# Kernel tuning notes

Hardware: AMD Instinct MI355X
Metric: run time of the kernel (lower is better)

Reference implementation:

```python
import jax, jax.numpy as jnp
import numpy as np

N_NODES = 50000
NEG_SLOPE = 0.2  # PyG GATConv default leaky-relu slope


def _gat_conv(x, edge_index, W, a_src, a_dst, bias, heads, out_ch, concat, num_nodes):
    # x: [N, F_in]; W: [F_in, heads*out_ch]; a_src/a_dst: [heads, out_ch]; bias: [heads*out_ch] or [out_ch]
    h = (x @ W).reshape(num_nodes, heads, out_ch)            # [N,H,C]
    alpha_src = jnp.einsum('nhc,hc->nh', h, a_src)           # [N,H]
    alpha_dst = jnp.einsum('nhc,hc->nh', h, a_dst)           # [N,H]
    src, dst = edge_index[0], edge_index[1]
    e = jax.nn.leaky_relu(alpha_src[src] + alpha_dst[dst], NEG_SLOPE)  # [E,H]
    # segment softmax over incoming edges per destination (self-loops guarantee non-empty segments)
    m = jax.ops.segment_max(e, dst, num_segments=num_nodes)
    e = jnp.exp(e - m[dst])
    denom = jax.ops.segment_sum(e, dst, num_segments=num_nodes)
    alpha = e / denom[dst]                                    # [E,H]
    msg = h[src] * alpha[:, :, None]                          # [E,H,C]
    out = jax.ops.segment_sum(msg, dst, num_segments=num_nodes)  # [N,H,C]
    if concat:
        out = out.reshape(num_nodes, heads * out_ch)
    else:
        out = out.mean(axis=1)
    return out + bias


def _add_self_loops(edge_index, num_nodes):
    loops = jnp.arange(num_nodes, dtype=edge_index.dtype)
    return jnp.concatenate([edge_index, jnp.stack([loops, loops])], axis=1)


def setup_inputs() -> dict:
    key = jax.random.key(0)
    ks = jax.random.split(key, 16)
    N, F_in, H, C_hid, C_out = N_NODES, 128, 4, 64, 64
    E = 800000
    x = jax.random.normal(ks[0], (N, F_in), dtype=jnp.float32)
    edge_index = jax.random.randint(ks[1], (2, E), 0, N, dtype=jnp.int32)
    s = lambda fan: 1.0 / np.sqrt(fan)
    inp = {
        'x': x, 'edge_index': edge_index,
        'W1': jax.random.normal(ks[2], (F_in, H * C_hid), jnp.float32) * s(F_in),
        'a_src1': jax.random.normal(ks[3], (H, C_hid), jnp.float32) * s(C_hid),
        'a_dst1': jax.random.normal(ks[4], (H, C_hid), jnp.float32) * s(C_hid),
        'b1': jnp.zeros((H * C_hid,), jnp.float32),
        'W2': jax.random.normal(ks[5], (H * C_hid, H * C_hid), jnp.float32) * s(H * C_hid),
        'a_src2': jax.random.normal(ks[6], (H, C_hid), jnp.float32) * s(C_hid),
        'a_dst2': jax.random.normal(ks[7], (H, C_hid), jnp.float32) * s(C_hid),
        'b2': jnp.zeros((H * C_hid,), jnp.float32),
        'W3': jax.random.normal(ks[8], (H * C_hid, C_out), jnp.float32) * s(H * C_hid),
        'a_src3': jax.random.normal(ks[9], (1, C_out), jnp.float32) * s(C_out),
        'a_dst3': jax.random.normal(ks[10], (1, C_out), jnp.float32) * s(C_out),
        'b3': jnp.zeros((C_out,), jnp.float32),
    }
    return inp


def reference(x, edge_index, W1, a_src1, a_dst1, b1, W2, a_src2, a_dst2, b2, W3, a_src3, a_dst3, b3):
    N = x.shape[0]
    ei = _add_self_loops(edge_index, N)
    h = _gat_conv(x, ei, W1, a_src1, a_dst1, b1, heads=4, out_ch=64, concat=True, num_nodes=N)
    h = jax.nn.elu(h)
    h = _gat_conv(h, ei, W2, a_src2, a_dst2, b2, heads=4, out_ch=64, concat=True, num_nodes=N)
    h = jax.nn.elu(h)
    out = _gat_conv(h, ei, W3, a_src3, a_dst3, b3, heads=1, out_ch=64, concat=False, num_nodes=N)
    return out
```

## Files before the change

### kernel.cpp

```cpp
#include <hip/hip_runtime.h>
#include <hip/hip_fp16.h>
#include <cstdint>


typedef _Float16 f16;
typedef _Float16 f16x8 __attribute__((ext_vector_type(8)));
typedef float f32x4 __attribute__((ext_vector_type(4)));

__global__ __launch_bounds__(256) void count_kernel(const int* __restrict__ ei,
                                                    int E, int N,
                                                    int* __restrict__ deg) {
  int g = blockIdx.x * 256 + threadIdx.x;
  if (g >= E + N) return;
  int dst = (g < E) ? ei[E + g] : (g - E);
  atomicAdd(&deg[dst], 1);
}

__global__ __launch_bounds__(256) void deg_block_reduce(const int* __restrict__ deg,
                                                        int* __restrict__ bsum, int N) {
  __shared__ int red[4];
  int b = blockIdx.x;
  int v = 0;
#pragma unroll
  for (int s = 0; s < 4; ++s) {
    int idx = b * 1024 + s * 256 + threadIdx.x;
    if (idx < N) v += deg[idx];
  }
  for (int off = 32; off; off >>= 1) v += __shfl_down(v, off);
  if ((threadIdx.x & 63) == 0) red[threadIdx.x >> 6] = v;
  __syncthreads();
  if (threadIdx.x == 0) bsum[b] = red[0] + red[1] + red[2] + red[3];
}

__global__ __launch_bounds__(1024) void small_scan(const int* __restrict__ bsum,
                                                   int* __restrict__ bpre, int NB) {
  __shared__ int buf[1024];
  int v = (threadIdx.x < NB) ? bsum[threadIdx.x] : 0;
  buf[threadIdx.x] = v;
  __syncthreads();
  for (int off = 1; off < 1024; off <<= 1) {
    int tv = (threadIdx.x >= off) ? buf[threadIdx.x - off] : 0;
    __syncthreads();
    buf[threadIdx.x] += tv;
    __syncthreads();
  }
  if (threadIdx.x < NB) bpre[threadIdx.x] = buf[threadIdx.x] - v;
}

__global__ __launch_bounds__(1024) void scan_final(const int* __restrict__ deg,
                                                   const int* __restrict__ bpre,
                                                   int* __restrict__ row_off,
                                                   int* __restrict__ cursor,
                                                   int N, int total) {
  __shared__ int buf[1024];
  int b = blockIdx.x;
  int i = b * 1024 + threadIdx.x;
  int v = (i < N) ? deg[i] : 0;
  buf[threadIdx.x] = v;
  __syncthreads();
  for (int off = 1; off < 1024; off <<= 1) {
    int tv = (threadIdx.x >= off) ? buf[threadIdx.x - off] : 0;
    __syncthreads();
    buf[threadIdx.x] += tv;
    __syncthreads();
  }
  if (i < N) {
    int ro = bpre[b] + buf[threadIdx.x] - v;
    row_off[i] = ro;
    cursor[i] = ro;
  }
  if (i == 0) row_off[N] = total;
}

__global__ __launch_bounds__(256) void scatter_kernel(const int* __restrict__ ei,
                                                      int E, int N,
                                                      int* __restrict__ cursor,
                                                      int* __restrict__ esrc,
                                                      int* __restrict__ edst) {
  int g = blockIdx.x * 256 + threadIdx.x;
  if (g >= E + N) return;
  int src, dst;
  if (g < E) { src = ei[g]; dst = ei[E + g]; }
  else       { src = g - E; dst = src; }
  int pos = atomicAdd(&cursor[dst], 1);
  esrc[pos] = src;
  edst[pos] = dst;
}

__global__ __launch_bounds__(256) void convert_all(
    const float* __restrict__ x, const float* __restrict__ W1,
    const float* __restrict__ W2, const float* __restrict__ W3,
    f16* __restrict__ xh, f16* __restrict__ Wt1, f16* __restrict__ Wt2,
    f16* __restrict__ Wt3, int nx4, int n1, int n2, int n3) {
  int t = blockIdx.x * 256 + threadIdx.x;
  if (t < nx4) {
    float4 v = *reinterpret_cast<const float4*>(&x[t * 4]);
    f16 o[4] = {(f16)v.x, (f16)v.y, (f16)v.z, (f16)v.w};
    *reinterpret_cast<uint2*>(&xh[t * 4]) = *reinterpret_cast<uint2*>(o);
    return;
  }
  t -= nx4;
  if (t < n1) {
    int n = t % 256, k = t / 256;
    Wt1[(size_t)n * 128 + k] = (f16)W1[t];
    return;
  }
  t -= n1;
  if (t < n2) {
    int n = t % 256, k = t / 256;
    int kp = (k & 192) | ((k & 15) << 2) | ((k >> 4) & 3);
    Wt2[(size_t)n * 256 + kp] = (f16)W2[t];
    return;
  }
  t -= n2;
  if (t < n3) {
    int n = t % 64, k = t / 64;
    int kp = (k & 192) | ((k & 15) << 2) | ((k >> 4) & 3);
    Wt3[(size_t)n * 256 + kp] = (f16)W3[t];
  }
}

template <int BN>
__global__ __launch_bounds__(256) void mfma_gemm_alpha(
    const f16* __restrict__ A, const f16* __restrict__ Bt,
    f16* __restrict__ Tout,
    const float* __restrict__ avec_src, const float* __restrict__ avec_dst,
    float* __restrict__ asrc, float* __restrict__ adst,
    int M, int K, int Ncol) {
  constexpr int RF = (BN == 128) ? 4 : 2;
  __shared__ f16 As[128][40];
  __shared__ f16 Bs[BN][40];
  int tid = threadIdx.x;
  int wv = tid >> 6, lane = tid & 63;
  int lrow = lane & 15, lkb = lane >> 4;
  int row0 = blockIdx.x * 128, col0 = blockIdx.y * BN;
  int wro = (BN == 128) ? (wv >> 1) * 64 : wv * 32;
  int wco = (BN == 128) ? (wv & 1) * 64 : 0;
  int hg = (col0 + wco) >> 6;

  f32x4 acc[RF][4];
#pragma unroll
  for (int rf = 0; rf < RF; ++rf)
#pragma unroll
    for (int cf = 0; cf < 4; ++cf) acc[rf][cf] = (f32x4){0.f, 0.f, 0.f, 0.f};

  for (int kk = 0; kk < K; kk += 32) {
#pragma unroll
    for (int q = 0; q < 2; ++q) {
      int slot = tid + q * 256;
      int r = slot >> 2, ko = (slot & 3) << 3;
      int gr = min(row0 + r, M - 1);
      *reinterpret_cast<f16x8*>(&As[r][ko]) =
          *reinterpret_cast<const f16x8*>(&A[(size_t)gr * K + kk + ko]);
    }
#pragma unroll
    for (int q = 0; q < BN / 64; ++q) {
      int slot = tid + q * 256;
      int c = slot >> 2, ko = (slot & 3) << 3;
      *reinterpret_cast<f16x8*>(&Bs[c][ko]) =
          *reinterpret_cast<const f16x8*>(&Bt[(size_t)(col0 + c) * K + kk + ko]);
    }
    __syncthreads();
    f16x8 af[RF], bf[4];
#pragma unroll
    for (int rf = 0; rf < RF; ++rf)
      af[rf] = *reinterpret_cast<f16x8*>(&As[wro + rf * 16 + lrow][lkb * 8]);
#pragma unroll
    for (int cf = 0; cf < 4; ++cf)
      bf[cf] = *reinterpret_cast<f16x8*>(&Bs[wco + cf * 16 + lrow][lkb * 8]);
#pragma unroll
    for (int rf = 0; rf < RF; ++rf)
#pragma unroll
      for (int cf = 0; cf < 4; ++cf)
        acc[rf][cf] = __builtin_amdgcn_mfma_f32_16x16x32_f16(af[rf], bf[cf],
                                                             acc[rf][cf], 0, 0, 0);
    __syncthreads();
  }

  int Hh = Ncol >> 6;
  float avs[4], avd[4];
#pragma unroll
  for (int cf = 0; cf < 4; ++cf) {
    avs[cf] = avec_src[hg * 64 + cf * 16 + lrow];
    avd[cf] = avec_dst[hg * 64 + cf * 16 + lrow];
  }

#pragma unroll
  for (int rf = 0; rf < RF; ++rf) {
#pragma unroll
    for (int r = 0; r < 4; ++r) {
      float ps = 0.f, pd = 0.f;
#pragma unroll
      for (int cf = 0; cf < 4; ++cf) {
        float v = acc[rf][cf][r];
        ps = fmaf(v, avs[cf], ps);
        pd = fmaf(v, avd[cf], pd);
      }
#pragma unroll
      for (int off = 1; off < 16; off <<= 1) {
        ps += __shfl_xor(ps, off);
        pd += __shfl_xor(pd, off);
      }
      int row = row0 + wro + rf * 16 + lkb * 4 + r;
      if (lrow == 0 && row < M) {
        asrc[row * Hh + hg] = ps;
        adst[row * Hh + hg] = pd;
      }
    }
#pragma unroll
    for (int r = 0; r < 4; ++r) {
      int row = row0 + wro + rf * 16 + lkb * 4 + r;
      if (row < M) {
        f16 o[4] = {(f16)acc[rf][0][r], (f16)acc[rf][1][r],
                    (f16)acc[rf][2][r], (f16)acc[rf][3][r]};
        *reinterpret_cast<uint2*>(
            &Tout[(size_t)row * Ncol + col0 + wco + (lrow << 2)]) =
            *reinterpret_cast<uint2*>(o);
      }
    }
  }
}

__global__ __launch_bounds__(256) void edge_weights_h4(
    const int* __restrict__ esrc, const int* __restrict__ edst,
    const float* __restrict__ asrc, const float* __restrict__ adst,
    float* __restrict__ w, int ET) {
  int t = blockIdx.x * 256 + threadIdx.x;
  if (t >= ET * 4) return;
  int j = t >> 2, h = t & 3;
  float e = asrc[esrc[j] * 4 + h] + adst[edst[j] * 4 + h];
  e = fmaxf(e, 0.2f * e);
  w[t] = __expf(e);
}

__global__ __launch_bounds__(256) void edge_weights_h1(
    const int* __restrict__ esrc, const int* __restrict__ edst,
    const float* __restrict__ asrc, const float* __restrict__ adst,
    float* __restrict__ w, int ET) {
  int j = blockIdx.x * 256 + threadIdx.x;
  if (j >= ET) return;
  float e = asrc[esrc[j]] + adst[edst[j]];
  e = fmaxf(e, 0.2f * e);
  w[j] = __expf(e);
}

template <bool ELU>
__global__ __launch_bounds__(256) void aggregate_h4(
    const f16* __restrict__ T16, const int* __restrict__ row_off,
    const int* __restrict__ esrc, const float* __restrict__ w,
    const float* __restrict__ bias, f16* __restrict__ outF, int N) {
  int wv = threadIdx.x >> 6, lane = threadIdx.x & 63;
  int dst = blockIdx.x * 4 + wv;
  if (dst >= N) return;
  int head = lane >> 4;
  int hsel = lane & 48;
  int r0 = row_off[dst], r1 = row_off[dst + 1];
  const char* tbase = reinterpret_cast<const char*>(T16);
  uint loff = (uint)lane * 8;
  float den = 0.f, ax = 0.f, ay = 0.f, az = 0.f, aw = 0.f;
  for (int base = r0; base < r1; base += 8) {
    int jb = base + (lane & 7);
    int sv = 0;
    float wl = 0.f;
    if (jb < r1) {
      sv = esrc[jb];
      wl = w[(jb << 2) + head];
    }
#pragma unroll
    for (int i = 0; i < 8; ++i) {
      int sj = __shfl(sv, i);
      float wj = __shfl(wl, hsel + i);
      den += wj;
      uint2 raw = *reinterpret_cast<const uint2*>(tbase + (((uint)sj << 9) + loff));
      __half2 p0 = *reinterpret_cast<__half2*>(&raw.x);
      __half2 p1 = *reinterpret_cast<__half2*>(&raw.y);
      float2 f0 = __half22float2(p0);
      float2 f1 = __half22float2(p1);
      ax = fmaf(wj, f0.x, ax);
      ay = fmaf(wj, f0.y, ay);
      az = fmaf(wj, f1.x, az);
      aw = fmaf(wj, f1.y, aw);
    }
  }
  float rd = 1.f / den;
  int l = lane & 15;
  int bb = hsel * 4 + l;
  float vx = ax * rd + bias[bb];
  float vy = ay * rd + bias[bb + 16];
  float vz = az * rd + bias[bb + 32];
  float vw = aw * rd + bias[bb + 48];
  if (ELU) {
    vx = vx > 0.f ? vx : expm1f(vx);
    vy = vy > 0.f ? vy : expm1f(vy);
    vz = vz > 0.f ? vz : expm1f(vz);
    vw = vw > 0.f ? vw : expm1f(vw);
  }
  f16 o[4] = {(f16)vx, (f16)vy, (f16)vz, (f16)vw};
  *reinterpret_cast<uint2*>(&outF[(size_t)dst * 256 + (lane << 2)]) =
      *reinterpret_cast<uint2*>(o);
}

__global__ __launch_bounds__(256) void aggregate_h1(
    const f16* __restrict__ T16, const int* __restrict__ row_off,
    const int* __restrict__ esrc, const float* __restrict__ w,
    const float* __restrict__ bias, float* __restrict__ out, int N) {
  int wv = threadIdx.x >> 6, lane = threadIdx.x & 63;
  int grp = lane >> 4, l = lane & 15;
  int gsel = lane & 48;
  int dst = blockIdx.x * 16 + wv * 4 + grp;
  if (dst >= N) return;
  int r0 = row_off[dst], r1 = row_off[dst + 1];
  const char* tbase = reinterpret_cast<const char*>(T16);
  uint loff = (uint)l * 8;
  float den = 0.f, ax = 0.f, ay = 0.f, az = 0.f, aw = 0.f;
  for (int base = r0; base < r1; base += 8) {
    int jb = base + (l & 7);
    int sv = 0;
    float wl = 0.f;
    if (jb < r1) {
      sv = esrc[jb];
      wl = w[jb];
    }
#pragma unroll
    for (int i = 0; i < 8; ++i) {
      int sj = __shfl(sv, gsel + i);
      float wj = __shfl(wl, gsel + i);
      den += wj;
      uint2 raw = *reinterpret_cast<const uint2*>(tbase + (((uint)sj << 7) + loff));
      __half2 p0 = *reinterpret_cast<__half2*>(&raw.x);
      __half2 p1 = *reinterpret_cast<__half2*>(&raw.y);
      float2 f0 = __half22float2(p0);
      float2 f1 = __half22float2(p1);
      ax = fmaf(wj, f0.x, ax);
      ay = fmaf(wj, f0.y, ay);
      az = fmaf(wj, f1.x, az);
      aw = fmaf(wj, f1.y, aw);
    }
  }
  float rd = 1.f / den;
  out[(size_t)dst * 64 + l]      = ax * rd + bias[l];
  out[(size_t)dst * 64 + 16 + l] = ay * rd + bias[16 + l];
  out[(size_t)dst * 64 + 32 + l] = az * rd + bias[32 + l];
  out[(size_t)dst * 64 + 48 + l] = aw * rd + bias[48 + l];
}

extern "C" void kernel_launch(void* const* d_in, const int* in_sizes, int n_in,
                              void* d_out, int out_size, void* d_ws, size_t ws_size,
                              hipStream_t stream) {
  const float* x   = (const float*)d_in[0];
  const int*   ei  = (const int*)d_in[1];
  const float* W1  = (const float*)d_in[2];
  const float* as1 = (const float*)d_in[3];
  const float* ad1 = (const float*)d_in[4];
  const float* b1  = (const float*)d_in[5];
  const float* W2  = (const float*)d_in[6];
  const float* as2 = (const float*)d_in[7];
  const float* ad2 = (const float*)d_in[8];
  const float* b2  = (const float*)d_in[9];
  const float* W3  = (const float*)d_in[10];
  const float* as3 = (const float*)d_in[11];
  const float* ad3 = (const float*)d_in[12];
  const float* b3  = (const float*)d_in[13];
  float* out = (float*)d_out;

  const int Fin = 128, H = 4, C = 64, HC = H * C;
  const int N = in_sizes[0] / Fin;
  const int E = in_sizes[1] / 2;
  const int ET = E + N;
  const int NB = (N + 1023) / 1024;

  f16* xh    = (f16*)d_ws;
  f16* T16   = xh + (size_t)N * Fin;
  f16* F16   = T16 + (size_t)N * HC;
  f16* T16L3 = F16 + (size_t)N * HC;
  f16* Wt1   = T16L3 + (size_t)N * C;
  f16* Wt2   = Wt1 + HC * Fin;
  f16* Wt3   = Wt2 + HC * HC;
  float* asrc = (float*)(Wt3 + C * HC);
  float* adst = asrc + (size_t)N * H;
  float* wbuf = adst + (size_t)N * H;
  int* deg     = (int*)(wbuf + (size_t)ET * 4);
  int* row_off = deg + N;
  int* cursor  = row_off + (N + 1);
  int* bsum    = cursor + N;
  int* bpre    = bsum + NB;
  int* esrc    = bpre + NB;
  int* edst    = esrc + ET;

  hipMemsetAsync(deg, 0, N * sizeof(int), stream);
  count_kernel<<<(ET + 255) / 256, 256, 0, stream>>>(ei, E, N, deg);
  deg_block_reduce<<<NB, 256, 0, stream>>>(deg, bsum, N);
  small_scan<<<1, 1024, 0, stream>>>(bsum, bpre, NB);
  scan_final<<<NB, 1024, 0, stream>>>(deg, bpre, row_off, cursor, N, ET);
  scatter_kernel<<<(ET + 255) / 256, 256, 0, stream>>>(ei, E, N, cursor, esrc, edst);

  int nx4 = N * Fin / 4;
  int n1 = Fin * HC, n2 = HC * HC, n3 = HC * C;
  convert_all<<<(nx4 + n1 + n2 + n3 + 255) / 256, 256, 0, stream>>>(
      x, W1, W2, W3, xh, Wt1, Wt2, Wt3, nx4, n1, n2, n3);

  int gx = (N + 127) / 128;
  int eb4 = (ET * 4 + 255) / 256, eb1 = (ET + 255) / 256;
  int ab4 = (N + 3) / 4;
  int ab1 = (N + 15) / 16;

  mfma_gemm_alpha<128><<<dim3(gx, 2), 256, 0, stream>>>(
      xh, Wt1, T16, as1, ad1, asrc, adst, N, Fin, HC);
  edge_weights_h4<<<eb4, 256, 0, stream>>>(esrc, edst, asrc, adst, wbuf, ET);
  aggregate_h4<true><<<ab4, 256, 0, stream>>>(T16, row_off, esrc, wbuf, b1, F16, N);

  mfma_gemm_alpha<128><<<dim3(gx, 2), 256, 0, stream>>>(
      F16, Wt2, T16, as2, ad2, asrc, adst, N, HC, HC);
  edge_weights_h4<<<eb4, 256, 0, stream>>>(esrc, edst, asrc, adst, wbuf, ET);
  aggregate_h4<true><<<ab4, 256, 0, stream>>>(T16, row_off, esrc, wbuf, b2, F16, N);

  mfma_gemm_alpha<64><<<dim3(gx, 1), 256, 0, stream>>>(
      F16, Wt3, T16L3, as3, ad3, asrc, adst, N, HC, C);
  edge_weights_h1<<<eb1, 256, 0, stream>>>(esrc, edst, asrc, adst, wbuf, ET);
  aggregate_h1<<<ab1, 256, 0, stream>>>(T16L3, row_off, esrc, wbuf, b3, out, N);
}
```

Measured before the change: 328.7 us.

## Balance h4 aggregation by splitting edges evenly across wavefronts

Replaces the one-wavefront-per-destination aggregation for the 4-head layers with an edge-balanced scheme. Each wavefront takes a contiguous range of about 64 edges, uses binary search on row offsets to find the destinations whose segments start in that range, and flushes each destination's result when its segment ends. This targets load imbalance from varying in-degrees and the idle lanes on short segments. In exchange it adds binary searches per wavefront and a per-edge boundary check inside the inner loop.

```diff
diff --git a/kernel.cpp b/kernel.cpp
--- a/kernel.cpp
+++ b/kernel.cpp
@@ -245,29 +245,67 @@
 }
 
 template <bool ELU>
-__global__ __launch_bounds__(256) void aggregate_h4(
+__global__ __launch_bounds__(256) void aggregate_h4_stream(
     const f16* __restrict__ T16, const int* __restrict__ row_off,
     const int* __restrict__ esrc, const float* __restrict__ w,
-    const float* __restrict__ bias, f16* __restrict__ outF, int N) {
+    const float* __restrict__ bias, f16* __restrict__ outF,
+    int N, int ET, int NW) {
   int wv = threadIdx.x >> 6, lane = threadIdx.x & 63;
-  int dst = blockIdx.x * 4 + wv;
-  if (dst >= N) return;
+  int wid = blockIdx.x * 4 + wv;
+  if (wid >= NW) return;
   int head = lane >> 4;
   int hsel = lane & 48;
-  int r0 = row_off[dst], r1 = row_off[dst + 1];
+  int l = lane & 15;
+  int t0 = (int)(((long long)wid * ET) / NW);
+  int t1 = (int)(((long long)(wid + 1) * ET) / NW);
+  int lo = 0, hi = N;
+  while (lo < hi) { int m = (lo + hi) >> 1; if (row_off[m] < t0) lo = m + 1; else hi = m; }
+  int d0 = lo;
+  lo = d0; hi = N;
+  while (lo < hi) { int m = (lo + hi) >> 1; if (row_off[m] < t1) lo = m + 1; else hi = m; }
+  int d1 = lo;
+  if (d0 >= d1) return;
+  int e0 = row_off[d0], e1 = row_off[d1];
+  int cd = d0;
+  int cend = row_off[d0 + 1];
   const char* tbase = reinterpret_cast<const char*>(T16);
   uint loff = (uint)lane * 8;
+  int bb = hsel * 4 + l;
+  float b0 = bias[bb], b1 = bias[bb + 16], b2 = bias[bb + 32], b3 = bias[bb + 48];
   float den = 0.f, ax = 0.f, ay = 0.f, az = 0.f, aw = 0.f;
-  for (int base = r0; base < r1; base += 8) {
+
+  auto flush = [&](int d) {
+    float rd = 1.f / den;
+    float vx = ax * rd + b0, vy = ay * rd + b1;
+    float vz = az * rd + b2, vw = aw * rd + b3;
+    if (ELU) {
+      vx = vx > 0.f ? vx : expm1f(vx);
+      vy = vy > 0.f ? vy : expm1f(vy);
+      vz = vz > 0.f ? vz : expm1f(vz);
+      vw = vw > 0.f ? vw : expm1f(vw);
+    }
+    f16 o[4] = {(f16)vx, (f16)vy, (f16)vz, (f16)vw};
+    *reinterpret_cast<uint2*>(&outF[(size_t)d * 256 + (lane << 2)]) =
+        *reinterpret_cast<uint2*>(o);
+    den = 0.f; ax = 0.f; ay = 0.f; az = 0.f; aw = 0.f;
+  };
+
+  for (int base = e0; base < e1; base += 8) {
     int jb = base + (lane & 7);
     int sv = 0;
     float wl = 0.f;
-    if (jb < r1) {
+    if (jb < e1) {
       sv = esrc[jb];
       wl = w[(jb << 2) + head];
     }
 #pragma unroll
     for (int i = 0; i < 8; ++i) {
+      int gj = base + i;
+      if (gj == cend) {
+        flush(cd);
+        ++cd;
+        cend = (cd < d1) ? row_off[cd + 1] : 0x7FFFFFFF;
+      }
       int sj = __shfl(sv, i);
       float wj = __shfl(wl, hsel + i);
       den += wj;
@@ -282,22 +320,7 @@
       aw = fmaf(wj, f1.y, aw);
     }
   }
-  float rd = 1.f / den;
-  int l = lane & 15;
-  int bb = hsel * 4 + l;
-  float vx = ax * rd + bias[bb];
-  float vy = ay * rd + bias[bb + 16];
-  float vz = az * rd + bias[bb + 32];
-  float vw = aw * rd + bias[bb + 48];
-  if (ELU) {
-    vx = vx > 0.f ? vx : expm1f(vx);
-    vy = vy > 0.f ? vy : expm1f(vy);
-    vz = vz > 0.f ? vz : expm1f(vz);
-    vw = vw > 0.f ? vw : expm1f(vw);
-  }
-  f16 o[4] = {(f16)vx, (f16)vy, (f16)vz, (f16)vw};
-  *reinterpret_cast<uint2*>(&outF[(size_t)dst * 256 + (lane << 2)]) =
-      *reinterpret_cast<uint2*>(o);
+  if (cd < d1) flush(cd);
 }
 
 __global__ __launch_bounds__(256) void aggregate_h1(
@@ -401,18 +424,21 @@
 
   int gx = (N + 127) / 128;
   int eb4 = (ET * 4 + 255) / 256, eb1 = (ET + 255) / 256;
-  int ab4 = (N + 3) / 4;
+  int NW = (ET + 63) / 64;
+  int abs4 = (NW + 3) / 4;
   int ab1 = (N + 15) / 16;
 
   mfma_gemm_alpha<128><<<dim3(gx, 2), 256, 0, stream>>>(
       xh, Wt1, T16, as1, ad1, asrc, adst, N, Fin, HC);
   edge_weights_h4<<<eb4, 256, 0, stream>>>(esrc, edst, asrc, adst, wbuf, ET);
-  aggregate_h4<true><<<ab4, 256, 0, stream>>>(T16, row_off, esrc, wbuf, b1, F16, N);
+  aggregate_h4_stream<true><<<abs4, 256, 0, stream>>>(
+      T16, row_off, esrc, wbuf, b1, F16, N, ET, NW);
 
   mfma_gemm_alpha<128><<<dim3(gx, 2), 256, 0, stream>>>(
       F16, Wt2, T16, as2, ad2, asrc, adst, N, HC, HC);
   edge_weights_h4<<<eb4, 256, 0, stream>>>(esrc, edst, asrc, adst, wbuf, ET);
-  aggregate_h4<true><<<ab4, 256, 0, stream>>>(T16, row_off, esrc, wbuf, b2, F16, N);
+  aggregate_h4_stream<true><<<abs4, 256, 0, stream>>>(
+      T16, row_off, esrc, wbuf, b2, F16, N, ET, NW);
 
   mfma_gemm_alpha<64><<<dim3(gx, 1), 256, 0, stream>>>(
       F16, Wt3, T16L3, as3, ad3, asrc, adst, N, HC, C);
```

Result: slower. 402.6 us (+22.5%).
